# Performance work log

Hardware: AMD Instinct MI355X
Metric: run time of the kernel (lower is better)

Reference implementation:

```python
import jax, jax.numpy as jnp
import numpy as np

# Dimensions (see shape_source): k=4 -> hk=cobj_size=2
K_LEVEL = 4
HK = K_LEVEL // 2            # conv kernel/stride, == cobj_size
BS = 16                      # MBS*ncobj groups
NUM_TOP = 512
BAG = 50                     # bag size B (orig_fea.shape[1])
D = 512                      # feature dim
H = 512                      # relation-unit hidden dim


def setup_inputs() -> dict:
    key = jax.random.key(0)
    ks = jax.random.split(key, 7)
    orig_fea = jax.random.normal(ks[0], (BS * 2 * HK, BAG, D), jnp.float32)
    ind0 = jax.random.randint(ks[1], (BS, NUM_TOP, HK), 0, BAG, jnp.int32)
    ind1 = jax.random.randint(ks[2], (BS, NUM_TOP, HK), 0, BAG, jnp.int32)
    W0 = jax.random.normal(ks[3], (D, H), jnp.float32) * 0.05
    W1 = jax.random.normal(ks[4], (D, H), jnp.float32) * 0.05
    b = jax.random.normal(ks[5], (H,), jnp.float32) * 0.05
    v = jax.random.normal(ks[6], (H,), jnp.float32) * 0.05
    return {"orig_fea": orig_fea, "ind0": ind0, "ind1": ind1,
            "W0": W0, "W1": W1, "b": b, "v": v}


def reference(orig_fea, ind0, ind1, W0, W1, b, v):
    bs = ind0.shape[0]
    bag = orig_fea.shape[1]
    cobj = ind0.shape[-1]                 # == k//2 == conv kernel hk
    d = orig_fea.shape[-1]

    # create_ids: offset by bag * position so ids index into the flattened half
    offs = (bag * jnp.arange(cobj)).astype(ind0.dtype)
    ids0 = (ind0 + offs).reshape(bs, -1)  # [bs, S], S = num_top*cobj
    ids1 = (ind1 + offs).reshape(bs, -1)

    # rsolo_fea: [bs, 2, X, D] with X = bag*cobj
    fea = orig_fea.reshape(bs, 2, -1, d)

    # relation unit over ALL X*X candidate pairs (dedupe+gather-back in the
    # original is pure memoization; compute-then-gather is the same math)
    h0 = jnp.einsum('bxd,dh->bxh', fea[:, 0], W0)   # [bs, X, H]
    h1 = jnp.einsum('byd,dh->byh', fea[:, 1], W1)   # [bs, X, H]
    hid = jax.nn.relu(h0[:, :, None, :] + h1[:, None, :, :] + b)  # [bs, X, X, H]
    full = jnp.einsum('bxyh,h->bxy', hid, v)        # [bs, X, X]

    # gather rows by ids0, cols by ids1 (per group)
    scores = jax.vmap(lambda f, i0, i1: f[i0][:, i1])(full, ids0, ids1)  # [bs, S, S]

    # Conv2D(1, kernel=hk, stride=hk, ones kernel, zero bias) == block sum-pool
    S = scores.shape[1]
    hk = cobj
    pooled = scores.reshape(bs, S // hk, hk, S // hk, hk).sum(axis=(2, 4))  # [bs, nt, nt]
    out_scores = pooled.reshape(bs, -1, 1)          # [bs, nt*nt, 1]

    nt0, nt1 = ind0.shape[1], ind1.shape[1]
    gi, gj = jnp.meshgrid(jnp.arange(nt0, dtype=jnp.int32),
                          jnp.arange(nt1, dtype=jnp.int32), indexing='ij')
    pairs = jnp.broadcast_to(jnp.stack([gi, gj], axis=-1)[None],
                             (bs, nt0, nt1, 2)).reshape(bs, nt0 * nt1, 2)
    return out_scores, pairs
```

## Files before the change

kernel.cpp:

```cpp
#include <hip/hip_runtime.h>

#define NBS   32
#define XDIM  100
#define DDIM  512
#define HDIM  512
#define NT    512
#define WS_WT 0
#define WS_H  1048576
#define WS_FP 7602176

typedef _Float16 half8 __attribute__((ext_vector_type(8)));
typedef float floatx4 __attribute__((ext_vector_type(4)));

__global__ void prep_w(const float* __restrict__ W0, const float* __restrict__ W1,
                       _Float16* __restrict__ Wt) {
    int o = blockIdx.x * 256 + threadIdx.x;
    int w = o >> 18;
    int rem = o & 262143;
    int c = rem >> 9;
    int d = rem & 511;
    const float* W = w ? W1 : W0;
    Wt[o] = (_Float16)W[d * 512 + c];
}

__global__ void __launch_bounds__(256) gemm_k(const float* __restrict__ fea,
                                              const _Float16* __restrict__ Wt,
                                              const float* __restrict__ bias,
                                              float* __restrict__ h) {
    int bx   = blockIdx.x;
    int bs   = bx / 14;
    int rem  = bx % 14;
    int rt   = rem >> 1;
    int chal = rem & 1;
    int w    = threadIdx.x >> 6;
    int lane = threadIdx.x & 63;
    int cg   = chal * 4 + w;
    int n0   = cg * 64;
    int m0   = rt * 16;
    int s    = bs & 1;
    int l15  = lane & 15;
    int q    = lane >> 4;

    const float* arow = fea + (size_t)bs * (XDIM * DDIM)
                        + (size_t)min(m0 + l15, XDIM - 1) * DDIM + q * 8;
    const _Float16* bbase = Wt + (size_t)s * (HDIM * DDIM) + q * 8;
    const _Float16* b0p = bbase + (size_t)(n0 +  0 + l15) * DDIM;
    const _Float16* b1p = bbase + (size_t)(n0 + 16 + l15) * DDIM;
    const _Float16* b2p = bbase + (size_t)(n0 + 32 + l15) * DDIM;
    const _Float16* b3p = bbase + (size_t)(n0 + 48 + l15) * DDIM;

    floatx4 acc0 = {0.f, 0.f, 0.f, 0.f};
    floatx4 acc1 = acc0, acc2 = acc0, acc3 = acc0;

    for (int k = 0; k < DDIM; k += 32) {
        float4 a0 = *(const float4*)(arow + k);
        float4 a1 = *(const float4*)(arow + k + 4);
        half8 af;
        af[0] = (_Float16)a0.x; af[1] = (_Float16)a0.y;
        af[2] = (_Float16)a0.z; af[3] = (_Float16)a0.w;
        af[4] = (_Float16)a1.x; af[5] = (_Float16)a1.y;
        af[6] = (_Float16)a1.z; af[7] = (_Float16)a1.w;
        half8 bf0 = *(const half8*)(b0p + k);
        half8 bf1 = *(const half8*)(b1p + k);
        half8 bf2 = *(const half8*)(b2p + k);
        half8 bf3 = *(const half8*)(b3p + k);
        acc0 = __builtin_amdgcn_mfma_f32_16x16x32_f16(af, bf0, acc0, 0, 0, 0);
        acc1 = __builtin_amdgcn_mfma_f32_16x16x32_f16(af, bf1, acc1, 0, 0, 0);
        acc2 = __builtin_amdgcn_mfma_f32_16x16x32_f16(af, bf2, acc2, 0, 0, 0);
        acc3 = __builtin_amdgcn_mfma_f32_16x16x32_f16(af, bf3, acc3, 0, 0, 0);
    }

    float* hb = h + (size_t)bs * (XDIM * HDIM);
    #pragma unroll
    for (int j = 0; j < 4; ++j) {
        floatx4 a = (j == 0) ? acc0 : (j == 1) ? acc1 : (j == 2) ? acc2 : acc3;
        int col = n0 + 16 * j + l15;
        float bi = s ? bias[col] : 0.f;
        #pragma unroll
        for (int r = 0; r < 4; ++r) {
            int m = m0 + q * 4 + r;
            if (m < XDIM) hb[(size_t)m * HDIM + col] = a[r] + bi;
        }
    }
}

__global__ void __launch_bounds__(256) full_k(const float* __restrict__ h,
                                              const float* __restrict__ v,
                                              float* __restrict__ fp) {
    int bx = blockIdx.x;
    int ks = bx >> 8;
    int rem = bx & 255;
    int b  = rem >> 4;
    int xt = (rem >> 2) & 3;
    int yt = rem & 3;
    int x0 = xt * 32, y0 = yt * 32;

    __shared__ float sh0[32][68];
    __shared__ float sh1[32][68];
    __shared__ float sv[64];

    int t  = threadIdx.x;
    int lx = (t >> 4) * 2;
    int ly = (t & 15) * 2;
    float acc00 = 0.f, acc01 = 0.f, acc10 = 0.f, acc11 = 0.f;

    const float* h0b = h + (size_t)(b * 2 + 0) * (XDIM * HDIM);
    const float* h1b = h + (size_t)(b * 2 + 1) * (XDIM * HDIM);

    for (int c = 0; c < 4; ++c) {
        int kc = ks * 256 + c * 64;
        if (c) __syncthreads();
        #pragma unroll
        for (int i = 0; i < 2; ++i) {
            int f = t + i * 256;
            int row = f >> 4, qq = f & 15;
            int gx = min(x0 + row, XDIM - 1);
            int gy = min(y0 + row, XDIM - 1);
            *(float4*)&sh0[row][qq * 4] = *(const float4*)(h0b + (size_t)gx * HDIM + kc + qq * 4);
            *(float4*)&sh1[row][qq * 4] = *(const float4*)(h1b + (size_t)gy * HDIM + kc + qq * 4);
        }
        if (t < 16) *(float4*)&sv[t * 4] = *(const float4*)(v + kc + t * 4);
        __syncthreads();

        for (int k = 0; k < 64; k += 4) {
            float4 a0 = *(const float4*)&sh0[lx][k];
            float4 a1 = *(const float4*)&sh0[lx + 1][k];
            float4 b0 = *(const float4*)&sh1[ly][k];
            float4 b1 = *(const float4*)&sh1[ly + 1][k];
            float4 vv = *(const float4*)&sv[k];
            const float* pa0 = (const float*)&a0;
            const float* pa1 = (const float*)&a1;
            const float* pb0 = (const float*)&b0;
            const float* pb1 = (const float*)&b1;
            const float* pv  = (const float*)&vv;
            #pragma unroll
            for (int j = 0; j < 4; ++j) {
                float vj = pv[j];
                acc00 += fmaxf(pa0[j] + pb0[j], 0.f) * vj;
                acc01 += fmaxf(pa0[j] + pb1[j], 0.f) * vj;
                acc10 += fmaxf(pa1[j] + pb0[j], 0.f) * vj;
                acc11 += fmaxf(pa1[j] + pb1[j], 0.f) * vj;
            }
        }
    }

    float* out = fp + ((size_t)ks * 16 + b) * (XDIM * XDIM);
    int x = x0 + lx, y = y0 + ly;
    if (x < XDIM) {
        if (y     < XDIM) out[(size_t)x * XDIM + y    ] = acc00;
        if (y + 1 < XDIM) out[(size_t)x * XDIM + y + 1] = acc01;
    }
    if (x + 1 < XDIM) {
        if (y     < XDIM) out[(size_t)(x + 1) * XDIM + y    ] = acc10;
        if (y + 1 < XDIM) out[(size_t)(x + 1) * XDIM + y + 1] = acc11;
    }
}

__global__ void __launch_bounds__(256) score_k(const float* __restrict__ fp,
                                               const int* __restrict__ ind0,
                                               const int* __restrict__ ind1,
                                               float* __restrict__ out) {
    int bx = blockIdx.x;
    int b  = bx >> 4;
    int i0 = (bx & 15) * 32;

    __shared__ float rowsum[32][100];
    __shared__ int c0s[NT], c1s[NT];
    __shared__ int a0s[32], a1s[32];

    int t = threadIdx.x;
    if (t < 32) {
        int2 ii = *(const int2*)(ind0 + ((size_t)b * NT + i0 + t) * 2);
        a0s[t] = ii.x;
        a1s[t] = ii.y + 50;
    }
    for (int j = t; j < NT; j += 256) {
        int2 jj = *(const int2*)(ind1 + ((size_t)b * NT + j) * 2);
        c0s[j] = jj.x;
        c1s[j] = jj.y + 50;
    }
    __syncthreads();

    const float* f0 = fp + (size_t)b * (XDIM * XDIM);
    const float* f1 = fp + (size_t)(16 + b) * (XDIM * XDIM);
    for (int idx = t; idx < 32 * 128; idx += 256) {
        int il = idx >> 7, y = idx & 127;
        if (y < XDIM) {
            int a0 = a0s[il], a1 = a1s[il];
            rowsum[il][y] = f0[a0 * XDIM + y] + f0[a1 * XDIM + y]
                          + f1[a0 * XDIM + y] + f1[a1 * XDIM + y];
        }
    }
    __syncthreads();

    float*  sout = out + (size_t)b * (NT * NT) + (size_t)i0 * NT;
    float2* pout = (float2*)(out + (size_t)16 * NT * NT
                             + (size_t)b * (NT * NT * 2) + (size_t)i0 * NT * 2);
    for (int o = t; o < 32 * NT; o += 256) {
        int il = o >> 9, j = o & 511;
        float sc = rowsum[il][c0s[j]] + rowsum[il][c1s[j]];
        sout[(size_t)il * NT + j] = sc;
        float2 pr;
        pr.x = (float)(i0 + il);
        pr.y = (float)j;
        pout[o] = pr;
    }
}

extern "C" void kernel_launch(void* const* d_in, const int* in_sizes, int n_in,
                              void* d_out, int out_size, void* d_ws, size_t ws_size,
                              hipStream_t stream) {
    const float* fea  = (const float*)d_in[0];
    const int*   ind0 = (const int*)d_in[1];
    const int*   ind1 = (const int*)d_in[2];
    const float* W0   = (const float*)d_in[3];
    const float* W1   = (const float*)d_in[4];
    const float* bias = (const float*)d_in[5];
    const float* v    = (const float*)d_in[6];
    float* out = (float*)d_out;
    char*  ws  = (char*)d_ws;

    _Float16* Wt = (_Float16*)(ws + WS_WT);
    float*    h  = (float*)(ws + WS_H);
    float*    fp = (float*)(ws + WS_FP);

    hipLaunchKernelGGL(prep_w,  dim3(2048), dim3(256), 0, stream, W0, W1, Wt);
    hipLaunchKernelGGL(gemm_k,  dim3(448),  dim3(256), 0, stream, fea, Wt, bias, h);
    hipLaunchKernelGGL(full_k,  dim3(512),  dim3(256), 0, stream, h, v, fp);
    hipLaunchKernelGGL(score_k, dim3(256),  dim3(256), 0, stream, fp, ind0, ind1, out);
}
```

Baseline: 139.8 us.

## Move relation unit to packed fp16 math with dot2 and retile kernels

Converts features, weights and v to fp16 in a combined prep kernel, stores hidden activations as fp16, and rewrites the pairwise relu-dot kernel to use packed half2 adds, max and fdot2 with 4x4 register tiles over 8 K-splits. The weight layout is reblocked for contiguous MFMA B loads. Writing the pair-index output moves into full_k, and score_k is split over column halves and sums 8 partial planes. This reduces memory traffic and ALU work but lowers precision of the hidden sums to fp16 and adds a larger partial-sum reduction.

```diff
diff --git a/kernel.cpp b/kernel.cpp
--- a/kernel.cpp
+++ b/kernel.cpp
@@ -1,76 +1,88 @@
 #include <hip/hip_runtime.h>
 
-#define NBS   32
 #define XDIM  100
 #define DDIM  512
 #define HDIM  512
 #define NT    512
-#define WS_WT 0
-#define WS_H  1048576
-#define WS_FP 7602176
-
-typedef _Float16 half8 __attribute__((ext_vector_type(8)));
-typedef float floatx4 __attribute__((ext_vector_type(4)));
-
-__global__ void prep_w(const float* __restrict__ W0, const float* __restrict__ W1,
-                       _Float16* __restrict__ Wt) {
-    int o = blockIdx.x * 256 + threadIdx.x;
-    int w = o >> 18;
-    int rem = o & 262143;
-    int c = rem >> 9;
-    int d = rem & 511;
-    const float* W = w ? W1 : W0;
-    Wt[o] = (_Float16)W[d * 512 + c];
-}
-
-__global__ void __launch_bounds__(256) gemm_k(const float* __restrict__ fea,
-                                              const _Float16* __restrict__ Wt,
+#define WS_WT2   0
+#define WS_FEA16 1048576
+#define WS_V16   4325376
+#define WS_H16   4326400
+#define WS_FP    7603200
+
+typedef _Float16 h16x8 __attribute__((ext_vector_type(8)));
+typedef _Float16 h2    __attribute__((ext_vector_type(2)));
+typedef float floatx4  __attribute__((ext_vector_type(4)));
+
+union H8U { h16x8 v; h2 p[4]; unsigned u[4]; };
+
+__global__ void __launch_bounds__(256) prep_k(const float* __restrict__ W0,
+                                              const float* __restrict__ W1,
+                                              const float* __restrict__ fea,
+                                              const float* __restrict__ v,
+                                              _Float16* __restrict__ Wt2,
+                                              _Float16* __restrict__ fea16,
+                                              _Float16* __restrict__ v16) {
+    int blk = blockIdx.x;
+    int t = threadIdx.x;
+    if (blk < 2048) {
+        int o  = blk * 256 + t;
+        int w  = o >> 18;
+        int kb = (o >> 14) & 15;
+        int c  = (o >> 5) & 511;
+        int qj = o & 31;
+        int d  = kb * 32 + qj;
+        const float* W = w ? W1 : W0;
+        Wt2[o] = (_Float16)W[d * 512 + c];
+    } else if (blk < 3648) {
+        int tid = (blk - 2048) * 256 + t;
+        float4 x = *(const float4*)(fea + (size_t)tid * 4);
+        _Float16 r[4] = {(_Float16)x.x, (_Float16)x.y, (_Float16)x.z, (_Float16)x.w};
+        *(uint2*)(fea16 + (size_t)tid * 4) = *(const uint2*)r;
+    } else {
+        v16[t * 2]     = (_Float16)v[t * 2];
+        v16[t * 2 + 1] = (_Float16)v[t * 2 + 1];
+    }
+}
+
+__global__ void __launch_bounds__(256) gemm_k(const _Float16* __restrict__ fea16,
+                                              const _Float16* __restrict__ Wt2,
                                               const float* __restrict__ bias,
-                                              float* __restrict__ h) {
+                                              _Float16* __restrict__ h16) {
     int bx   = blockIdx.x;
-    int bs   = bx / 14;
+    int hb   = bx / 14;
     int rem  = bx % 14;
     int rt   = rem >> 1;
     int chal = rem & 1;
     int w    = threadIdx.x >> 6;
     int lane = threadIdx.x & 63;
-    int cg   = chal * 4 + w;
-    int n0   = cg * 64;
+    int n0   = (chal * 4 + w) * 64;
     int m0   = rt * 16;
-    int s    = bs & 1;
+    int s    = hb & 1;
     int l15  = lane & 15;
     int q    = lane >> 4;
-
-    const float* arow = fea + (size_t)bs * (XDIM * DDIM)
-                        + (size_t)min(m0 + l15, XDIM - 1) * DDIM + q * 8;
-    const _Float16* bbase = Wt + (size_t)s * (HDIM * DDIM) + q * 8;
-    const _Float16* b0p = bbase + (size_t)(n0 +  0 + l15) * DDIM;
-    const _Float16* b1p = bbase + (size_t)(n0 + 16 + l15) * DDIM;
-    const _Float16* b2p = bbase + (size_t)(n0 + 32 + l15) * DDIM;
-    const _Float16* b3p = bbase + (size_t)(n0 + 48 + l15) * DDIM;
+    int m    = min(m0 + l15, XDIM - 1);
+
+    const _Float16* ap = fea16 + (size_t)hb * (XDIM * DDIM) + (size_t)m * DDIM + q * 8;
+    const _Float16* bp = Wt2 + (size_t)s * 262144 + (size_t)(n0 + l15) * 32 + q * 8;
 
     floatx4 acc0 = {0.f, 0.f, 0.f, 0.f};
     floatx4 acc1 = acc0, acc2 = acc0, acc3 = acc0;
 
-    for (int k = 0; k < DDIM; k += 32) {
-        float4 a0 = *(const float4*)(arow + k);
-        float4 a1 = *(const float4*)(arow + k + 4);
-        half8 af;
-        af[0] = (_Float16)a0.x; af[1] = (_Float16)a0.y;
-        af[2] = (_Float16)a0.z; af[3] = (_Float16)a0.w;
-        af[4] = (_Float16)a1.x; af[5] = (_Float16)a1.y;
-        af[6] = (_Float16)a1.z; af[7] = (_Float16)a1.w;
-        half8 bf0 = *(const half8*)(b0p + k);
-        half8 bf1 = *(const half8*)(b1p + k);
-        half8 bf2 = *(const half8*)(b2p + k);
-        half8 bf3 = *(const half8*)(b3p + k);
-        acc0 = __builtin_amdgcn_mfma_f32_16x16x32_f16(af, bf0, acc0, 0, 0, 0);
-        acc1 = __builtin_amdgcn_mfma_f32_16x16x32_f16(af, bf1, acc1, 0, 0, 0);
-        acc2 = __builtin_amdgcn_mfma_f32_16x16x32_f16(af, bf2, acc2, 0, 0, 0);
-        acc3 = __builtin_amdgcn_mfma_f32_16x16x32_f16(af, bf3, acc3, 0, 0, 0);
-    }
-
-    float* hb = h + (size_t)bs * (XDIM * HDIM);
+    for (int kb = 0; kb < 16; ++kb) {
+        h16x8 a = *(const h16x8*)(ap + kb * 32);
+        const _Float16* bkb = bp + kb * 16384;
+        h16x8 b0 = *(const h16x8*)(bkb);
+        h16x8 b1 = *(const h16x8*)(bkb + 512);
+        h16x8 b2 = *(const h16x8*)(bkb + 1024);
+        h16x8 b3 = *(const h16x8*)(bkb + 1536);
+        acc0 = __builtin_amdgcn_mfma_f32_16x16x32_f16(a, b0, acc0, 0, 0, 0);
+        acc1 = __builtin_amdgcn_mfma_f32_16x16x32_f16(a, b1, acc1, 0, 0, 0);
+        acc2 = __builtin_amdgcn_mfma_f32_16x16x32_f16(a, b2, acc2, 0, 0, 0);
+        acc3 = __builtin_amdgcn_mfma_f32_16x16x32_f16(a, b3, acc3, 0, 0, 0);
+    }
+
+    _Float16* hob = h16 + (size_t)hb * (XDIM * HDIM);
     #pragma unroll
     for (int j = 0; j < 4; ++j) {
         floatx4 a = (j == 0) ? acc0 : (j == 1) ? acc1 : (j == 2) ? acc2 : acc3;
@@ -78,81 +90,104 @@
         float bi = s ? bias[col] : 0.f;
         #pragma unroll
         for (int r = 0; r < 4; ++r) {
-            int m = m0 + q * 4 + r;
-            if (m < XDIM) hb[(size_t)m * HDIM + col] = a[r] + bi;
-        }
-    }
-}
-
-__global__ void __launch_bounds__(256) full_k(const float* __restrict__ h,
-                                              const float* __restrict__ v,
-                                              float* __restrict__ fp) {
-    int bx = blockIdx.x;
-    int ks = bx >> 8;
-    int rem = bx & 255;
-    int b  = rem >> 4;
-    int xt = (rem >> 2) & 3;
-    int yt = rem & 3;
-    int x0 = xt * 32, y0 = yt * 32;
-
-    __shared__ float sh0[32][68];
-    __shared__ float sh1[32][68];
-    __shared__ float sv[64];
-
-    int t  = threadIdx.x;
-    int lx = (t >> 4) * 2;
-    int ly = (t & 15) * 2;
-    float acc00 = 0.f, acc01 = 0.f, acc10 = 0.f, acc11 = 0.f;
-
-    const float* h0b = h + (size_t)(b * 2 + 0) * (XDIM * HDIM);
-    const float* h1b = h + (size_t)(b * 2 + 1) * (XDIM * HDIM);
-
-    for (int c = 0; c < 4; ++c) {
-        int kc = ks * 256 + c * 64;
-        if (c) __syncthreads();
-        #pragma unroll
-        for (int i = 0; i < 2; ++i) {
-            int f = t + i * 256;
-            int row = f >> 4, qq = f & 15;
-            int gx = min(x0 + row, XDIM - 1);
-            int gy = min(y0 + row, XDIM - 1);
-            *(float4*)&sh0[row][qq * 4] = *(const float4*)(h0b + (size_t)gx * HDIM + kc + qq * 4);
-            *(float4*)&sh1[row][qq * 4] = *(const float4*)(h1b + (size_t)gy * HDIM + kc + qq * 4);
-        }
-        if (t < 16) *(float4*)&sv[t * 4] = *(const float4*)(v + kc + t * 4);
-        __syncthreads();
-
-        for (int k = 0; k < 64; k += 4) {
-            float4 a0 = *(const float4*)&sh0[lx][k];
-            float4 a1 = *(const float4*)&sh0[lx + 1][k];
-            float4 b0 = *(const float4*)&sh1[ly][k];
-            float4 b1 = *(const float4*)&sh1[ly + 1][k];
-            float4 vv = *(const float4*)&sv[k];
-            const float* pa0 = (const float*)&a0;
-            const float* pa1 = (const float*)&a1;
-            const float* pb0 = (const float*)&b0;
-            const float* pb1 = (const float*)&b1;
-            const float* pv  = (const float*)&vv;
+            int mr = m0 + q * 4 + r;
+            if (mr < XDIM) hob[(size_t)mr * HDIM + col] = (_Float16)(a[r] + bi);
+        }
+    }
+}
+
+__global__ void __launch_bounds__(256) full_k(const _Float16* __restrict__ h16,
+                                              const _Float16* __restrict__ v16,
+                                              float* __restrict__ fp,
+                                              float2* __restrict__ pout) {
+    int bx  = blockIdx.x;
+    int ks  = bx >> 6;
+    int rem = bx & 63;
+    int b   = rem >> 2;
+    int xt  = (rem >> 1) & 1;
+    int yt  = rem & 1;
+    int x0  = xt * 36;
+    int y0  = yt * 36;
+    int kc  = ks * 64;
+
+    __shared__ _Float16 sh0[64][72];
+    __shared__ unsigned sh1p[32][64];
+    __shared__ unsigned sv[32];
+
+    int t = threadIdx.x;
+    int r = t & 63, kseg = t >> 6;
+
+    const _Float16* g0 = h16 + ((size_t)(b * 2) * XDIM + x0 + r) * HDIM + kc + kseg * 16;
+    *(h16x8*)&sh0[r][kseg * 16]     = *(const h16x8*)g0;
+    *(h16x8*)&sh0[r][kseg * 16 + 8] = *(const h16x8*)(g0 + 8);
+
+    const _Float16* g1 = h16 + ((size_t)(b * 2 + 1) * XDIM + y0 + r) * HDIM + kc + kseg * 16;
+    H8U u0, u1;
+    u0.v = *(const h16x8*)g1;
+    u1.v = *(const h16x8*)(g1 + 8);
+    #pragma unroll
+    for (int pp = 0; pp < 4; ++pp) {
+        sh1p[kseg * 8 + pp][r]     = u0.u[pp];
+        sh1p[kseg * 8 + 4 + pp][r] = u1.u[pp];
+    }
+    if (t < 32) sv[t] = *(const unsigned*)(v16 + kc + t * 2);
+    __syncthreads();
+
+    {
+        size_t pbase = (size_t)bx * 8192;
+        #pragma unroll 4
+        for (int i = 0; i < 32; ++i) {
+            unsigned idx = (unsigned)(pbase + i * 256 + t);
+            float2 pr;
+            pr.x = (float)((idx >> 9) & 511);
+            pr.y = (float)(idx & 511);
+            pout[idx] = pr;
+        }
+    }
+
+    int ty = t >> 4, tx = t & 15;
+    float acc[4][4] = {};
+    h2 hz; hz[0] = (_Float16)0; hz[1] = (_Float16)0;
+
+    for (int kk = 0; kk < 8; ++kk) {
+        H8U a[4];
+        #pragma unroll
+        for (int i = 0; i < 4; ++i)
+            a[i].v = *(const h16x8*)&sh0[ty * 4 + i][kk * 8];
+        uint4 bq[4];
+        #pragma unroll
+        for (int p = 0; p < 4; ++p)
+            bq[p] = *(const uint4*)&sh1p[kk * 4 + p][tx * 4];
+        uint4 vq = *(const uint4*)&sv[kk * 4];
+        const unsigned* vqa = (const unsigned*)&vq;
+
+        #pragma unroll
+        for (int p = 0; p < 4; ++p) {
+            h2 vp = __builtin_bit_cast(h2, vqa[p]);
+            const unsigned* bqa = (const unsigned*)&bq[p];
             #pragma unroll
-            for (int j = 0; j < 4; ++j) {
-                float vj = pv[j];
-                acc00 += fmaxf(pa0[j] + pb0[j], 0.f) * vj;
-                acc01 += fmaxf(pa0[j] + pb1[j], 0.f) * vj;
-                acc10 += fmaxf(pa1[j] + pb0[j], 0.f) * vj;
-                acc11 += fmaxf(pa1[j] + pb1[j], 0.f) * vj;
+            for (int i = 0; i < 4; ++i) {
+                h2 av = a[i].p[p];
+                #pragma unroll
+                for (int j = 0; j < 4; ++j) {
+                    h2 s = av + __builtin_bit_cast(h2, bqa[j]);
+                    s = __builtin_elementwise_max(s, hz);
+#if __has_builtin(__builtin_amdgcn_fdot2)
+                    acc[i][j] = __builtin_amdgcn_fdot2(s, vp, acc[i][j], false);
+#else
+                    acc[i][j] += (float)s[0] * (float)vp[0] + (float)s[1] * (float)vp[1];
+#endif
+                }
             }
         }
     }
 
-    float* out = fp + ((size_t)ks * 16 + b) * (XDIM * XDIM);
-    int x = x0 + lx, y = y0 + ly;
-    if (x < XDIM) {
-        if (y     < XDIM) out[(size_t)x * XDIM + y    ] = acc00;
-        if (y + 1 < XDIM) out[(size_t)x * XDIM + y + 1] = acc01;
-    }
-    if (x + 1 < XDIM) {
-        if (y     < XDIM) out[(size_t)(x + 1) * XDIM + y    ] = acc10;
-        if (y + 1 < XDIM) out[(size_t)(x + 1) * XDIM + y + 1] = acc11;
+    float* fpb = fp + (size_t)(ks * 16 + b) * (XDIM * XDIM);
+    #pragma unroll
+    for (int i = 0; i < 4; ++i) {
+        float4 o;
+        o.x = acc[i][0]; o.y = acc[i][1]; o.z = acc[i][2]; o.w = acc[i][3];
+        *(float4*)&fpb[(size_t)(x0 + ty * 4 + i) * XDIM + y0 + tx * 4] = o;
     }
 }
 
@@ -160,13 +195,16 @@
                                                const int* __restrict__ ind0,
                                                const int* __restrict__ ind1,
                                                float* __restrict__ out) {
-    int bx = blockIdx.x;
-    int b  = bx >> 4;
-    int i0 = (bx & 15) * 32;
+    int bx  = blockIdx.x;
+    int b   = bx >> 5;
+    int rem = bx & 31;
+    int it  = rem >> 1;
+    int jh  = rem & 1;
+    int i0  = it * 32;
 
     __shared__ float rowsum[32][100];
-    __shared__ int c0s[NT], c1s[NT];
     __shared__ int a0s[32], a1s[32];
+    __shared__ int c0s[256], c1s[256];
 
     int t = threadIdx.x;
     if (t < 32) {
@@ -174,36 +212,37 @@
         a0s[t] = ii.x;
         a1s[t] = ii.y + 50;
     }
-    for (int j = t; j < NT; j += 256) {
-        int2 jj = *(const int2*)(ind1 + ((size_t)b * NT + j) * 2);
-        c0s[j] = jj.x;
-        c1s[j] = jj.y + 50;
+    {
+        int2 jj = *(const int2*)(ind1 + ((size_t)b * NT + jh * 256 + t) * 2);
+        c0s[t] = jj.x;
+        c1s[t] = jj.y + 50;
     }
     __syncthreads();
 
-    const float* f0 = fp + (size_t)b * (XDIM * XDIM);
-    const float* f1 = fp + (size_t)(16 + b) * (XDIM * XDIM);
-    for (int idx = t; idx < 32 * 128; idx += 256) {
-        int il = idx >> 7, y = idx & 127;
-        if (y < XDIM) {
-            int a0 = a0s[il], a1 = a1s[il];
-            rowsum[il][y] = f0[a0 * XDIM + y] + f0[a1 * XDIM + y]
-                          + f1[a0 * XDIM + y] + f1[a1 * XDIM + y];
+    const float* fb = fp + (size_t)b * (XDIM * XDIM);
+    for (int idx = t; idx < 1024; idx += 256) {
+        int il = idx >> 5, yq = idx & 31;
+        if (yq < 25) {
+            float4 s = {0.f, 0.f, 0.f, 0.f};
+            int a0 = a0s[il] * XDIM + yq * 4;
+            int a1 = a1s[il] * XDIM + yq * 4;
+            #pragma unroll
+            for (int ksb = 0; ksb < 8; ++ksb) {
+                const float* pl = fb + (size_t)ksb * (16 * XDIM * XDIM);
+                float4 u = *(const float4*)(pl + a0);
+                float4 w = *(const float4*)(pl + a1);
+                s.x += u.x + w.x; s.y += u.y + w.y;
+                s.z += u.z + w.z; s.w += u.w + w.w;
+            }
+            *(float4*)&rowsum[il][yq * 4] = s;
         }
     }
     __syncthreads();
 
-    float*  sout = out + (size_t)b * (NT * NT) + (size_t)i0 * NT;
-    float2* pout = (float2*)(out + (size_t)16 * NT * NT
-                             + (size_t)b * (NT * NT * 2) + (size_t)i0 * NT * 2);
-    for (int o = t; o < 32 * NT; o += 256) {
-        int il = o >> 9, j = o & 511;
-        float sc = rowsum[il][c0s[j]] + rowsum[il][c1s[j]];
-        sout[(size_t)il * NT + j] = sc;
-        float2 pr;
-        pr.x = (float)(i0 + il);
-        pr.y = (float)j;
-        pout[o] = pr;
+    float* sout = out + (size_t)b * (NT * NT) + (size_t)i0 * NT + jh * 256;
+    for (int o = t; o < 8192; o += 256) {
+        int il = o >> 8, jl = o & 255;
+        sout[(size_t)il * NT + jl] = rowsum[il][c0s[jl]] + rowsum[il][c1s[jl]];
     }
 }
 
@@ -220,12 +259,15 @@
     float* out = (float*)d_out;
     char*  ws  = (char*)d_ws;
 
-    _Float16* Wt = (_Float16*)(ws + WS_WT);
-    float*    h  = (float*)(ws + WS_H);
-    float*    fp = (float*)(ws + WS_FP);
-
-    hipLaunchKernelGGL(prep_w,  dim3(2048), dim3(256), 0, stream, W0, W1, Wt);
-    hipLaunchKernelGGL(gemm_k,  dim3(448),  dim3(256), 0, stream, fea, Wt, bias, h);
-    hipLaunchKernelGGL(full_k,  dim3(512),  dim3(256), 0, stream, h, v, fp);
-    hipLaunchKernelGGL(score_k, dim3(256),  dim3(256), 0, stream, fp, ind0, ind1, out);
-}
+    _Float16* Wt2   = (_Float16*)(ws + WS_WT2);
+    _Float16* fea16 = (_Float16*)(ws + WS_FEA16);
+    _Float16* v16   = (_Float16*)(ws + WS_V16);
+    _Float16* h16   = (_Float16*)(ws + WS_H16);
+    float*    fp    = (float*)(ws + WS_FP);
+    float2*   pout  = (float2*)(out + (size_t)16 * NT * NT);
+
+    hipLaunchKernelGGL(prep_k,  dim3(3649), dim3(256), 0, stream, W0, W1, fea, v, Wt2, fea16, v16);
+    hipLaunchKernelGGL(gemm_k,  dim3(448),  dim3(256), 0, stream, fea16, Wt2, bias, h16);
+    hipLaunchKernelGGL(full_k,  dim3(512),  dim3(256), 0, stream, h16, v16, fp, pout);
+    hipLaunchKernelGGL(score_k, dim3(512),  dim3(256), 0, stream, fp, ind0, ind1, out);
+}
```

After: 122.0 us. -12.7%, faster.
